# Performance work log

Hardware: AMD Instinct MI355X
Metric: run time of the kernel (lower is better)

## Reference

```python
import jax, jax.numpy as jnp
import numpy as np

HIDDEN = 4096
N_HEADS = 32
HEAD_DIM = HIDDEN // N_HEADS
B = 8
S = 1024
N = B * S


def _build_cos_sin(max_pos, head_dim):
    inv_freq = 1.0 / (10000.0 ** (np.arange(0, head_dim, 2, dtype=np.float32) / head_dim))
    t = np.arange(max_pos, dtype=np.float32)
    freqs = np.outer(t, inv_freq)                 # [max_pos, head_dim/2]
    emb = np.concatenate([freqs, freqs], axis=-1)  # [max_pos, head_dim]
    return jnp.asarray(np.cos(emb)), jnp.asarray(np.sin(emb))


def setup_inputs() -> dict:
    key = jax.random.key(0)
    ks = jax.random.split(key, 5)
    cos, sin = _build_cos_sin(S, HEAD_DIM)
    scale = 0.02
    inp = {
        "cos": cos,
        "sin": sin,
        "nz_hidden_states": jax.random.normal(ks[0], (N, HIDDEN), jnp.float32),
        "nz_position_ids": jnp.tile(jnp.arange(S, dtype=jnp.int32), B),
        "cu_seqlens": jnp.arange(B + 1, dtype=jnp.int32) * S,
        "max_seqlen": S,
        "Wq": jax.random.normal(ks[1], (HIDDEN, HIDDEN), jnp.float32) * scale,
        "Wk": jax.random.normal(ks[2], (HIDDEN, HIDDEN), jnp.float32) * scale,
        "Wv": jax.random.normal(ks[3], (HIDDEN, HIDDEN), jnp.float32) * scale,
        "Wo": jax.random.normal(ks[4], (HIDDEN, HIDDEN), jnp.float32) * scale,
    }
    return inp


def _rotate_half(x):
    x1, x2 = jnp.split(x, 2, axis=-1)
    return jnp.concatenate([-x2, x1], axis=-1)


def reference(cos, sin, nz_hidden_states, nz_position_ids, cu_seqlens, max_seqlen, Wq, Wk, Wv, Wo):
    n_tok = nz_hidden_states.shape[0]
    b = cu_seqlens.shape[0] - 1
    s = n_tok // b  # equal-length packing
    h, d = N_HEADS, HEAD_DIM

    q = (nz_hidden_states @ Wq.T).reshape(n_tok, h, d)
    k = (nz_hidden_states @ Wk.T).reshape(n_tok, h, d)
    v = (nz_hidden_states @ Wv.T).reshape(n_tok, h, d)

    # RoPE: cos/sin gathered per token, broadcast over heads
    c = cos[nz_position_ids][:, None, :]  # [N,1,D]
    sn = sin[nz_position_ids][:, None, :]
    q = q * c + _rotate_half(q) * sn
    k = k * c + _rotate_half(k) * sn

    # Varlen causal attention (equal-length segments -> batch reshape)
    qb = q.reshape(b, s, h, d)
    kb = k.reshape(b, s, h, d)
    vb = v.reshape(b, s, h, d)
    scores = jnp.einsum('bqhd,bkhd->bhqk', qb, kb) / jnp.sqrt(jnp.float32(d))
    causal = jnp.tril(jnp.ones((s, s), dtype=bool))
    scores = jnp.where(causal, scores, jnp.finfo(scores.dtype).min)
    probs = jax.nn.softmax(scores, axis=-1)
    out = jnp.einsum('bhqk,bkhd->bqhd', probs, vb).reshape(n_tok, h * d)
    return out @ Wo.T
```

## Files before the change

kernel.cpp:

```cpp
#include <hip/hip_runtime.h>
#include <hip/hip_bf16.h>

#define NTOK 8192
#define HID 4096
#define NHEADS 32
#define HDIM 128
#define SEQ 1024
#define NSTEP (HID / 32)

typedef float f32x4 __attribute__((ext_vector_type(4)));
typedef short bf16x8 __attribute__((ext_vector_type(8)));

__device__ __forceinline__ ushort f2bf(float f) {
  union { float f; unsigned u; } x;
  x.f = f;
  unsigned r = x.u + 0x7fffu + ((x.u >> 16) & 1u);
  return (ushort)(r >> 16);
}
__device__ __forceinline__ float bf2f(ushort h) {
  union { unsigned u; float f; } x;
  x.u = ((unsigned)h) << 16;
  return x.f;
}

__global__ __launch_bounds__(256) void cvt_bf16_kernel(const float4* __restrict__ in,
                                                       ushort4* __restrict__ out, int n4) {
  int i = blockIdx.x * 256 + threadIdx.x;
  if (i < n4) {
    float4 v = in[i];
    ushort4 o;
    o.x = f2bf(v.x); o.y = f2bf(v.y); o.z = f2bf(v.z); o.w = f2bf(v.w);
    out[i] = o;
  }
}


__device__ __forceinline__ void gload16(const void* g, void* l) {
  __builtin_amdgcn_global_load_lds(
      (const __attribute__((address_space(1))) unsigned int*)g,
      (__attribute__((address_space(3))) unsigned int*)l, 16, 0, 0);
}

__device__ __forceinline__ void stage32(const ushort* gA, const ushort* gB,
                                        int rowA0, int rowB0, int k0,
                                        ushort* ldsA, ushort* ldsB, int tid) {
  const int wid = tid >> 6, lane = tid & 63;
#pragma unroll
  for (int q = 0; q < 2; ++q) {
    int wuni = q * 8192 + wid * 1024;
    int off = wuni + lane * 16;
    int row = off >> 6;
    int kb = (off ^ (((row >> 1) & 3) << 4)) & 63;
    gload16(gA + (size_t)(rowA0 + row) * HID + k0 + (kb >> 1), (char*)ldsA + wuni);
    gload16(gB + (size_t)(rowB0 + row) * HID + k0 + (kb >> 1), (char*)ldsB + wuni);
  }
}

#define GSTEP(T, DO_STAGE, VMC)                                                \
  do {                                                                         \
    const char* cA = (const char*)ringA[(T) & 3];                              \
    const char* cB = (const char*)ringB[(T) & 3];                              \
                                            \
    _Pragma("unroll") for (int ii = 0; ii < 4; ++ii) {                         \
      int L = (wm * 128 + ii * 16 + l15) * 64 + l4 * 16;                       \
      af[ii] = *(const bf16x8*)(cA + (L ^ swzr));                              \
    }                                                                          \
    _Pragma("unroll") for (int jj = 0; jj < 4; ++jj) {                         \
      int L = (wn * 64 + jj * 16 + l15) * 64 + l4 * 16;                        \
      bfr[jj] = *(const bf16x8*)(cB + (L ^ swzr));                             \
    }                                                                          \
    if (DO_STAGE)                                                              \
      stage32(Abf, Bp, m0, n0, ((T) + 3) * 32, ringA[((T) + 3) & 3],           \
              ringB[((T) + 3) & 3], tid);                                      \
    asm volatile("s_waitcnt lgkmcnt(0)" ::: "memory");                         \
    __builtin_amdgcn_sched_barrier(0);                                         \
    __builtin_amdgcn_s_setprio(1);                                             \
    _Pragma("unroll") for (int ii = 0; ii < 4; ++ii)                           \
        _Pragma("unroll") for (int jj = 0; jj < 4; ++jj)                       \
            acc[ii][jj] = __builtin_amdgcn_mfma_f32_16x16x32_bf16(             \
                af[ii], bfr[jj], acc[ii][jj], 0, 0, 0);                        \
    __builtin_amdgcn_s_setprio(0);                                             \
     \
    _Pragma("unroll") for (int ii = 0; ii < 4; ++ii) {                         \
      int L = (wm * 128 + (ii + 4) * 16 + l15) * 64 + l4 * 16;                 \
      af[ii] = *(const bf16x8*)(cA + (L ^ swzr));                              \
    }                                                                          \
    asm volatile("s_waitcnt lgkmcnt(0)" ::: "memory");                         \
    __builtin_amdgcn_sched_barrier(0);                                         \
    __builtin_amdgcn_s_setprio(1);                                             \
    _Pragma("unroll") for (int ii = 0; ii < 4; ++ii)                           \
        _Pragma("unroll") for (int jj = 0; jj < 4; ++jj)                       \
            acc[ii + 4][jj] = __builtin_amdgcn_mfma_f32_16x16x32_bf16(         \
                af[ii], bfr[jj], acc[ii + 4][jj], 0, 0, 0);                    \
    __builtin_amdgcn_s_setprio(0);                                             \
    if ((VMC) == 4) asm volatile("s_waitcnt vmcnt(4)" ::: "memory");           \
    else if ((VMC) == 0) asm volatile("s_waitcnt vmcnt(0)" ::: "memory");      \
    if ((VMC) >= 0) __builtin_amdgcn_s_barrier();                              \
  } while (0)

template <bool OUTF32>
__global__ __launch_bounds__(512, 2) void gemm256_kernel(
    const ushort* __restrict__ Abf,
    const ushort* __restrict__ B0, const ushort* __restrict__ B1,
    const ushort* __restrict__ B2,
    void* __restrict__ O0, void* __restrict__ O1, void* __restrict__ O2,
    int NTALL) {
  __shared__ __align__(16) ushort ringA[4][8192];
  __shared__ __align__(16) ushort ringB[4][8192];

  const int tid = threadIdx.x;
  const int l = tid & 63, wid = tid >> 6;
  const int wm = wid >> 2, wn = wid & 3;
  const int l15 = l & 15, l4 = l >> 4;
  const int swzr = ((l15 >> 1) & 3) << 4;

  const int nwg = gridDim.x;
  const int cpx = nwg >> 3;
  const int bid = blockIdx.x;
  const int lgid = (bid & 7) * cpx + (bid >> 3);
  const int bandw = NTALL << 3;
  const int band = lgid / bandw, rem = lgid % bandw;
  const int nt = rem >> 3;
  const int mt = (band << 3) + (rem & 7);
  const int m0 = mt * 256;
  const int sel = nt >> 4;
  const int n0 = (nt & 15) * 256;
  const ushort* Bp = (sel == 0) ? B0 : ((sel == 1) ? B1 : B2);
  void* Op = (sel == 0) ? O0 : ((sel == 1) ? O1 : O2);

  f32x4 acc[8][4];
  const f32x4 zero = {0.f, 0.f, 0.f, 0.f};
#pragma unroll
  for (int i = 0; i < 8; ++i)
#pragma unroll
    for (int j = 0; j < 4; ++j) acc[i][j] = zero;

  stage32(Abf, Bp, m0, n0, 0, ringA[0], ringB[0], tid);
  stage32(Abf, Bp, m0, n0, 32, ringA[1], ringB[1], tid);
  stage32(Abf, Bp, m0, n0, 64, ringA[2], ringB[2], tid);
  asm volatile("s_waitcnt vmcnt(4)" ::: "memory");
  __builtin_amdgcn_s_barrier();

  bf16x8 af[4], bfr[4];
  for (int tt = 0; tt < NSTEP - 4; tt += 4) {
    GSTEP(tt + 0, true, 4);
    GSTEP(tt + 1, true, 4);
    GSTEP(tt + 2, true, 4);
    GSTEP(tt + 3, true, 4);
  }
  GSTEP(NSTEP - 4, true, 4);
  GSTEP(NSTEP - 3, false, 0);
  GSTEP(NSTEP - 2, false, -1);
  GSTEP(NSTEP - 1, false, -1);

#pragma unroll
  for (int i = 0; i < 8; ++i) {
    const int row = m0 + wm * 128 + i * 16 + l4 * 4;
#pragma unroll
    for (int j = 0; j < 4; ++j) {
      const int col = n0 + wn * 64 + j * 16 + l15;
#pragma unroll
      for (int r = 0; r < 4; ++r) {
        float v = acc[i][j][r];
        if constexpr (OUTF32)
          ((float*)Op)[(size_t)(row + r) * HID + col] = v;
        else
          ((ushort*)Op)[(size_t)(row + r) * HID + col] = f2bf(v);
      }
    }
  }
}

template <bool ISBF>
__device__ __forceinline__ void stage_tile(ushort* lds, const void* gp, int row0, int k0, int tid) {
  if constexpr (ISBF) {
    const ushort* g = (const ushort*)gp;
#pragma unroll
    for (int i = 0; i < 2; ++i) {
      int row = (tid >> 2) + i * 64;
      int gr = tid & 3;
      bf16x8 v = *(const bf16x8*)(g + (size_t)(row0 + row) * HID + k0 + gr * 8);
      int gs = gr ^ ((row >> 1) & 3);
      *(bf16x8*)((char*)lds + row * 64 + gs * 16) = v;
    }
  } else {
    const float* g = (const float*)gp;
    int row = tid >> 1;
    const float* rp = g + (size_t)(row0 + row) * HID + k0;
#pragma unroll
    for (int i = 0; i < 2; ++i) {
      int gr = (tid & 1) * 2 + i;
      float4 a = *(const float4*)(rp + gr * 8);
      float4 b = *(const float4*)(rp + gr * 8 + 4);
      bf16x8 v;
      v[0] = (short)f2bf(a.x); v[1] = (short)f2bf(a.y);
      v[2] = (short)f2bf(a.z); v[3] = (short)f2bf(a.w);
      v[4] = (short)f2bf(b.x); v[5] = (short)f2bf(b.y);
      v[6] = (short)f2bf(b.z); v[7] = (short)f2bf(b.w);
      int gs = gr ^ ((row >> 1) & 3);
      *(bf16x8*)((char*)lds + row * 64 + gs * 16) = v;
    }
  }
}

template <bool ABF, bool BBF, bool OUTF32>
__global__ __launch_bounds__(256) void gemm_bt_kernel(
    const void* __restrict__ Ap,
    const void* __restrict__ B0, const void* __restrict__ B1, const void* __restrict__ B2,
    void* __restrict__ O0, void* __restrict__ O1, void* __restrict__ O2,
    int ntiles_per_w) {
  __shared__ __align__(16) ushort lA[128 * 32];
  __shared__ __align__(16) ushort lB[128 * 32];
  const int tid = threadIdx.x;
  const int l = tid & 63, wid = tid >> 6;
  const int wm = wid >> 1, wn = wid & 1;
  const int l15 = l & 15, l4 = l >> 4;
  const int mt0 = blockIdx.y * 128;
  const int ntile = blockIdx.x;
  const int sel = ntile / ntiles_per_w;
  const int nt0 = (ntile % ntiles_per_w) * 128;
  const void* Bp = (sel == 0) ? B0 : ((sel == 1) ? B1 : B2);
  void* Op = (sel == 0) ? O0 : ((sel == 1) ? O1 : O2);

  const f32x4 zero = {0.f, 0.f, 0.f, 0.f};
  f32x4 acc[4][4];
#pragma unroll
  for (int i = 0; i < 4; ++i)
#pragma unroll
    for (int j = 0; j < 4; ++j) acc[i][j] = zero;

  for (int k0 = 0; k0 < HID; k0 += 32) {
    stage_tile<ABF>(lA, Ap, mt0, k0, tid);
    stage_tile<BBF>(lB, Bp, nt0, k0, tid);
    __syncthreads();
    bf16x8 af[4], bfr[4];
#pragma unroll
    for (int i = 0; i < 4; ++i) {
      int rowa = wm * 64 + i * 16 + l15;
      int ga = l4 ^ ((rowa >> 1) & 3);
      af[i] = *(const bf16x8*)((const char*)lA + rowa * 64 + ga * 16);
      int rowb = wn * 64 + i * 16 + l15;
      int gb = l4 ^ ((rowb >> 1) & 3);
      bfr[i] = *(const bf16x8*)((const char*)lB + rowb * 64 + gb * 16);
    }
#pragma unroll
    for (int i = 0; i < 4; ++i)
#pragma unroll
      for (int j = 0; j < 4; ++j)
        acc[i][j] = __builtin_amdgcn_mfma_f32_16x16x32_bf16(af[i], bfr[j], acc[i][j], 0, 0, 0);
    __syncthreads();
  }

#pragma unroll
  for (int i = 0; i < 4; ++i) {
#pragma unroll
    for (int j = 0; j < 4; ++j) {
      int row = mt0 + wm * 64 + i * 16 + l4 * 4;
      int col = nt0 + wn * 64 + j * 16 + l15;
#pragma unroll
      for (int r = 0; r < 4; ++r) {
        float v = acc[i][j][r];
        if constexpr (OUTF32)
          ((float*)Op)[(size_t)(row + r) * HID + col] = v;
        else
          ((ushort*)Op)[(size_t)(row + r) * HID + col] = f2bf(v);
      }
    }
  }
}

__global__ __launch_bounds__(256) void rope_kernel(
    ushort* __restrict__ q, ushort* __restrict__ k,
    const float* __restrict__ cosT, const float* __restrict__ sinT,
    const int* __restrict__ pos) {
  int idx = blockIdx.x * 256 + threadIdx.x;
  int token = idx >> 8;
  int head = (idx >> 3) & 31;
  int c = idx & 7;
  int p = pos[token];
  size_t base = (size_t)token * HID + head * HDIM + c * 8;
  bf16x8 ql = *(bf16x8*)(q + base);
  bf16x8 qh = *(bf16x8*)(q + base + 64);
  bf16x8 kl = *(bf16x8*)(k + base);
  bf16x8 kh = *(bf16x8*)(k + base + 64);
  float4 c0 = *(const float4*)(cosT + (size_t)p * HDIM + c * 8);
  float4 c1 = *(const float4*)(cosT + (size_t)p * HDIM + c * 8 + 4);
  float4 s0 = *(const float4*)(sinT + (size_t)p * HDIM + c * 8);
  float4 s1 = *(const float4*)(sinT + (size_t)p * HDIM + c * 8 + 4);
  float cs[8] = {c0.x, c0.y, c0.z, c0.w, c1.x, c1.y, c1.z, c1.w};
  float sn[8] = {s0.x, s0.y, s0.z, s0.w, s1.x, s1.y, s1.z, s1.w};
  const float qsc = 0.08838834764831845f;
  bf16x8 qlo, qho, klo, kho;
#pragma unroll
  for (int j = 0; j < 8; ++j) {
    float qlf = bf2f((ushort)ql[j]), qhf = bf2f((ushort)qh[j]);
    float klf = bf2f((ushort)kl[j]), khf = bf2f((ushort)kh[j]);
    qlo[j] = (short)f2bf((qlf * cs[j] - qhf * sn[j]) * qsc);
    qho[j] = (short)f2bf((qhf * cs[j] + qlf * sn[j]) * qsc);
    klo[j] = (short)f2bf(klf * cs[j] - khf * sn[j]);
    kho[j] = (short)f2bf(khf * cs[j] + klf * sn[j]);
  }
  *(bf16x8*)(q + base) = qlo;
  *(bf16x8*)(q + base + 64) = qho;
  *(bf16x8*)(k + base) = klo;
  *(bf16x8*)(k + base + 64) = kho;
}

__global__ __launch_bounds__(256) void attn_kernel(
    const ushort* __restrict__ qb, const ushort* __restrict__ kb,
    const ushort* __restrict__ vb, ushort* __restrict__ ob) {
  __shared__ __align__(16) ushort lK[32 * 128];
  __shared__ __align__(16) ushort lVT[128 * 32];
  __shared__ __align__(16) ushort lP[4][16 * 32];

  const int tid = threadIdx.x;
  const int l = tid & 63, wid = tid >> 6;
  const int l15 = l & 15, l4 = l >> 4;
  const int q0 = blockIdx.x * 64;
  const int h = blockIdx.y;
  const size_t seqbase = (size_t)blockIdx.z * SEQ;

  bf16x8 qf[4];
  {
    const ushort* qp = qb + (seqbase + q0 + wid * 16 + l15) * HID + h * HDIM + l4 * 8;
#pragma unroll
    for (int kk = 0; kk < 4; ++kk) qf[kk] = *(const bf16x8*)(qp + kk * 32);
  }

  const f32x4 zero = {0.f, 0.f, 0.f, 0.f};
  f32x4 oacc[8];
#pragma unroll
  for (int t = 0; t < 8; ++t) oacc[t] = zero;
  float mrow[4] = {-3e38f, -3e38f, -3e38f, -3e38f};
  float lrow[4] = {0.f, 0.f, 0.f, 0.f};

  const int ntile = q0 / 32 + 2;
  for (int kt = 0; kt < ntile; ++kt) {
    const int k0 = kt * 32;
    {
      int r = tid >> 3;
      const ushort* kp = kb + (seqbase + k0 + r) * HID + h * HDIM;
#pragma unroll
      for (int i = 0; i < 2; ++i) {
        int g = (tid & 7) * 2 + i;
        bf16x8 kv = *(const bf16x8*)(kp + g * 8);
        int gs = g ^ (r & 7);
        *(bf16x8*)((char*)lK + r * 256 + gs * 16) = kv;
      }
    }
    {
      int d = tid & 127;
      int j0 = (tid >> 7) * 16;
      const ushort* vp = vb + (seqbase + k0 + j0) * HID + h * HDIM + d;
      ushort tmp[16];
#pragma unroll
      for (int j = 0; j < 16; ++j) tmp[j] = vp[(size_t)j * HID];
#pragma unroll
      for (int i = 0; i < 2; ++i) {
        bf16x8 vv;
#pragma unroll
        for (int jj = 0; jj < 8; ++jj) vv[jj] = (short)tmp[i * 8 + jj];
        int g = (j0 >> 3) + i;
        int gs = g ^ ((d >> 1) & 3);
        *(bf16x8*)((char*)lVT + d * 64 + gs * 16) = vv;
      }
    }
    __syncthreads();

    f32x4 s[2];
#pragma unroll
    for (int hf = 0; hf < 2; ++hf) {
      f32x4 c = zero;
      int row = hf * 16 + l15;
#pragma unroll
      for (int kk = 0; kk < 4; ++kk) {
        int gs = (kk * 4 + l4) ^ (row & 7);
        bf16x8 kf = *(const bf16x8*)((const char*)lK + row * 256 + gs * 16);
        c = __builtin_amdgcn_mfma_f32_16x16x32_bf16(qf[kk], kf, c, 0, 0, 0);
      }
      s[hf] = c;
    }

    const int qrow = q0 + wid * 16 + l4 * 4;
#pragma unroll
    for (int r = 0; r < 4; ++r) {
      float s0 = (k0 + l15 <= qrow + r) ? s[0][r] : -1e30f;
      float s1 = (k0 + 16 + l15 <= qrow + r) ? s[1][r] : -1e30f;
      float tmax = fmaxf(s0, s1);
#pragma unroll
      for (int off = 8; off; off >>= 1) tmax = fmaxf(tmax, __shfl_xor(tmax, off));
      float newm = fmaxf(mrow[r], tmax);
      float sc = __expf(mrow[r] - newm);
      float p0 = __expf(s0 - newm);
      float p1 = __expf(s1 - newm);
      float rs = p0 + p1;
#pragma unroll
      for (int off = 8; off; off >>= 1) rs += __shfl_xor(rs, off);
      lrow[r] = lrow[r] * sc + rs;
      mrow[r] = newm;
#pragma unroll
      for (int t = 0; t < 8; ++t) oacc[t][r] *= sc;
      lP[wid][(l4 * 4 + r) * 32 + l15] = f2bf(p0);
      lP[wid][(l4 * 4 + r) * 32 + 16 + l15] = f2bf(p1);
    }
    asm volatile("s_waitcnt lgkmcnt(0)" ::: "memory");
    __builtin_amdgcn_sched_barrier(0);

    bf16x8 pf = *(const bf16x8*)((const char*)&lP[wid][0] + l15 * 64 + l4 * 16);
#pragma unroll
    for (int t = 0; t < 8; ++t) {
      int d = t * 16 + l15;
      int gs = l4 ^ ((d >> 1) & 3);
      bf16x8 vf = *(const bf16x8*)((const char*)lVT + d * 64 + gs * 16);
      oacc[t] = __builtin_amdgcn_mfma_f32_16x16x32_bf16(pf, vf, oacc[t], 0, 0, 0);
    }
    __syncthreads();
  }

#pragma unroll
  for (int r = 0; r < 4; ++r) {
    float inv = 1.0f / lrow[r];
    ushort* op = ob + (seqbase + q0 + wid * 16 + l4 * 4 + r) * HID + h * HDIM + l15;
#pragma unroll
    for (int t = 0; t < 8; ++t) op[t * 16] = f2bf(oacc[t][r] * inv);
  }
}

extern "C" void kernel_launch(void* const* d_in, const int* in_sizes, int n_in,
                              void* d_out, int out_size, void* d_ws, size_t ws_size,
                              hipStream_t stream) {
  const float* cosT = (const float*)d_in[0];
  const float* sinT = (const float*)d_in[1];
  const float* X    = (const float*)d_in[2];
  const int*   pos  = (const int*)d_in[3];
  const float* Wq = (const float*)d_in[6];
  const float* Wk = (const float*)d_in[7];
  const float* Wv = (const float*)d_in[8];
  const float* Wo = (const float*)d_in[9];
  float* out = (float*)d_out;

  char* ws = (char*)d_ws;
  const size_t QKVB = (size_t)NTOK * HID * 2;
  const size_t WB = (size_t)HID * HID * 2;
  const size_t XB = QKVB;
  ushort* qbuf = (ushort*)(ws);
  ushort* kbuf = (ushort*)(ws + QKVB);
  ushort* vbuf = (ushort*)(ws + 2 * QKVB);

  dim3 blk(256);
  const int n4x = NTOK * HID / 4;
  const int n4w = HID * HID / 4;

  const bool fast = ws_size >= 3 * QKVB + XB + 4 * WB;
  const bool mid = !fast && ws_size >= 3 * QKVB + 2 * WB &&
                   (size_t)out_size * 4 >= XB + 2 * WB;

  if (fast || mid) {
    ushort *xb, *wqb, *wkb, *wvb, *wob;
    if (fast) {
      xb  = (ushort*)(ws + 3 * QKVB);
      wqb = (ushort*)(ws + 3 * QKVB + XB);
      wkb = (ushort*)(ws + 3 * QKVB + XB + WB);
      wvb = (ushort*)(ws + 3 * QKVB + XB + 2 * WB);
      wob = (ushort*)(ws + 3 * QKVB + XB + 3 * WB);
    } else {
      xb  = (ushort*)d_out;
      wqb = (ushort*)((char*)d_out + XB);
      wkb = (ushort*)((char*)d_out + XB + WB);
      wvb = (ushort*)(ws + 3 * QKVB);
      wob = (ushort*)(ws + 3 * QKVB + WB);
    }
    cvt_bf16_kernel<<<n4x / 256, blk, 0, stream>>>((const float4*)X, (ushort4*)xb, n4x);
    cvt_bf16_kernel<<<n4w / 256, blk, 0, stream>>>((const float4*)Wq, (ushort4*)wqb, n4w);
    cvt_bf16_kernel<<<n4w / 256, blk, 0, stream>>>((const float4*)Wk, (ushort4*)wkb, n4w);
    cvt_bf16_kernel<<<n4w / 256, blk, 0, stream>>>((const float4*)Wv, (ushort4*)wvb, n4w);
    cvt_bf16_kernel<<<n4w / 256, blk, 0, stream>>>((const float4*)Wo, (ushort4*)wob, n4w);
    gemm256_kernel<false><<<dim3(32 * 48), dim3(512), 0, stream>>>(
        xb, wqb, wkb, wvb, qbuf, kbuf, vbuf, 48);
    rope_kernel<<<NTOK * NHEADS * 8 / 256, blk, 0, stream>>>(qbuf, kbuf, cosT, sinT, pos);
    attn_kernel<<<dim3(16, 32, 8), blk, 0, stream>>>(qbuf, kbuf, vbuf, qbuf);
    gemm256_kernel<true><<<dim3(32 * 16), dim3(512), 0, stream>>>(
        qbuf, wob, wob, wob, out, out, out, 16);
  } else {
    gemm_bt_kernel<false, false, false><<<dim3(96, 64), blk, 0, stream>>>(
        X, Wq, Wk, Wv, qbuf, kbuf, vbuf, 32);
    rope_kernel<<<NTOK * NHEADS * 8 / 256, blk, 0, stream>>>(qbuf, kbuf, cosT, sinT, pos);
    attn_kernel<<<dim3(16, 32, 8), blk, 0, stream>>>(qbuf, kbuf, vbuf, qbuf);
    gemm_bt_kernel<true, false, true><<<dim3(32, 64), blk, 0, stream>>>(
        qbuf, Wo, Wo, Wo, out, out, out, 32);
  }
}
```

Baseline: 1.545 ms.

## Restructure GEMM pipeline to prefetch depth two with split A/B staging and extra barriers

Reduces the GEMM ring-buffer prefetch distance from three steps to two. A and B tile loads are now issued separately, interleaved between the two MFMA half-phases, with added workgroup barriers around each phase. The intent is to spread global-to-LDS traffic across the step and keep wave execution in lockstep. In exchange it adds three s_barriers per K step and leaves less latency hiding for global loads. The vmcnt(4) wait counts were not adjusted for the new load grouping, which may be wrong.

```diff
diff --git a/kernel.cpp b/kernel.cpp
--- a/kernel.cpp
+++ b/kernel.cpp
@@ -41,9 +41,8 @@
       (__attribute__((address_space(3))) unsigned int*)l, 16, 0, 0);
 }
 
-__device__ __forceinline__ void stage32(const ushort* gA, const ushort* gB,
-                                        int rowA0, int rowB0, int k0,
-                                        ushort* ldsA, ushort* ldsB, int tid) {
+__device__ __forceinline__ void stage_one(ushort* lds, const ushort* g,
+                                          int row0, int k0, int tid) {
   const int wid = tid >> 6, lane = tid & 63;
 #pragma unroll
   for (int q = 0; q < 2; ++q) {
@@ -51,16 +50,15 @@
     int off = wuni + lane * 16;
     int row = off >> 6;
     int kb = (off ^ (((row >> 1) & 3) << 4)) & 63;
-    gload16(gA + (size_t)(rowA0 + row) * HID + k0 + (kb >> 1), (char*)ldsA + wuni);
-    gload16(gB + (size_t)(rowB0 + row) * HID + k0 + (kb >> 1), (char*)ldsB + wuni);
-  }
-}
-
-#define GSTEP(T, DO_STAGE, VMC)                                                \
+    gload16(g + (size_t)(row0 + row) * HID + k0 + (kb >> 1), (char*)lds + wuni);
+  }
+}
+
+#define GSLOT(T, DO_STAGE, VMC)                                                \
   do {                                                                         \
     const char* cA = (const char*)ringA[(T) & 3];                              \
     const char* cB = (const char*)ringB[(T) & 3];                              \
-                                            \
+                       \
     _Pragma("unroll") for (int ii = 0; ii < 4; ++ii) {                         \
       int L = (wm * 128 + ii * 16 + l15) * 64 + l4 * 16;                       \
       af[ii] = *(const bf16x8*)(cA + (L ^ swzr));                              \
@@ -70,8 +68,8 @@
       bfr[jj] = *(const bf16x8*)(cB + (L ^ swzr));                             \
     }                                                                          \
     if (DO_STAGE)                                                              \
-      stage32(Abf, Bp, m0, n0, ((T) + 3) * 32, ringA[((T) + 3) & 3],           \
-              ringB[((T) + 3) & 3], tid);                                      \
+      stage_one(ringA[((T) + 2) & 3], Abf, m0, ((T) + 2) * 32, tid);           \
+    __builtin_amdgcn_s_barrier();                                              \
     asm volatile("s_waitcnt lgkmcnt(0)" ::: "memory");                         \
     __builtin_amdgcn_sched_barrier(0);                                         \
     __builtin_amdgcn_s_setprio(1);                                             \
@@ -80,11 +78,15 @@
             acc[ii][jj] = __builtin_amdgcn_mfma_f32_16x16x32_bf16(             \
                 af[ii], bfr[jj], acc[ii][jj], 0, 0, 0);                        \
     __builtin_amdgcn_s_setprio(0);                                             \
-     \
+    __builtin_amdgcn_s_barrier();                                              \
+                 \
     _Pragma("unroll") for (int ii = 0; ii < 4; ++ii) {                         \
       int L = (wm * 128 + (ii + 4) * 16 + l15) * 64 + l4 * 16;                 \
       af[ii] = *(const bf16x8*)(cA + (L ^ swzr));                              \
     }                                                                          \
+    if (DO_STAGE)                                                              \
+      stage_one(ringB[((T) + 2) & 3], Bp, n0, ((T) + 2) * 32, tid);            \
+    __builtin_amdgcn_s_barrier();                                              \
     asm volatile("s_waitcnt lgkmcnt(0)" ::: "memory");                         \
     __builtin_amdgcn_sched_barrier(0);                                         \
     __builtin_amdgcn_s_setprio(1);                                             \
@@ -135,23 +137,20 @@
 #pragma unroll
     for (int j = 0; j < 4; ++j) acc[i][j] = zero;
 
-  stage32(Abf, Bp, m0, n0, 0, ringA[0], ringB[0], tid);
-  stage32(Abf, Bp, m0, n0, 32, ringA[1], ringB[1], tid);
-  stage32(Abf, Bp, m0, n0, 64, ringA[2], ringB[2], tid);
+  stage_one(ringA[0], Abf, m0, 0, tid);
+  stage_one(ringB[0], Bp, n0, 0, tid);
+  stage_one(ringA[1], Abf, m0, 32, tid);
+  stage_one(ringB[1], Bp, n0, 32, tid);
   asm volatile("s_waitcnt vmcnt(4)" ::: "memory");
   __builtin_amdgcn_s_barrier();
 
   bf16x8 af[4], bfr[4];
-  for (int tt = 0; tt < NSTEP - 4; tt += 4) {
-    GSTEP(tt + 0, true, 4);
-    GSTEP(tt + 1, true, 4);
-    GSTEP(tt + 2, true, 4);
-    GSTEP(tt + 3, true, 4);
-  }
-  GSTEP(NSTEP - 4, true, 4);
-  GSTEP(NSTEP - 3, false, 0);
-  GSTEP(NSTEP - 2, false, -1);
-  GSTEP(NSTEP - 1, false, -1);
+  for (int tt = 0; tt < NSTEP - 2; tt += 2) {
+    GSLOT(tt + 0, true, 4);
+    GSLOT(tt + 1, (tt + 1 <= NSTEP - 3), 4);
+  }
+  GSLOT(NSTEP - 2, false, 0);
+  GSLOT(NSTEP - 1, false, -1);
 
 #pragma unroll
   for (int i = 0; i < 8; ++i) {
```

New measurement: 1.746 ms. +13.0%, slower.
